# Kernel optimization log

Measured on AMD Instinct MI355X. Metric: run time of the kernel, lower is better.

Reference implementation:

```python
import jax, jax.numpy as jnp
import numpy as np
import math

D_MODEL = 512
N_HEADS = 2
B, S = 2, 1024
THRESHOLD = 0.5  # kwargs default 'sparsity_threshold'


def setup_inputs() -> dict:
    key = jax.random.key(0)
    ks = jax.random.split(key, 10)
    D, H = D_MODEL, D_MODEL // 4
    std = 0.02
    return {
        "x": jax.random.normal(ks[0], (B, S, D), jnp.float32),
        "Wq": jax.random.normal(ks[1], (D, D), jnp.float32) * std,
        "Wk": jax.random.normal(ks[2], (D, D), jnp.float32) * std,
        "Wv": jax.random.normal(ks[3], (D, D), jnp.float32) * std,
        "Wo": jax.random.normal(ks[4], (D, D), jnp.float32) * std,
        "bo": jnp.zeros((D,), jnp.float32),
        "W1": jax.random.normal(ks[5], (D, H), jnp.float32) * std,
        "b1": jnp.zeros((H,), jnp.float32),
        "W2": jax.random.normal(ks[6], (H, 1), jnp.float32) * std,
        "b2": jnp.zeros((1,), jnp.float32),
    }


def reference(x, Wq, Wk, Wv, Wo, bo, W1, b1, W2, b2):
    Bsz, Seq, D = x.shape
    Hn = N_HEADS
    dh = D // Hn

    def split_heads(t):
        return t.reshape(Bsz, Seq, Hn, dh).transpose(0, 2, 1, 3)  # [B,H,S,dh]

    q = split_heads(x @ Wq)
    k = split_heads(x @ Wk)
    v = split_heads(x @ Wv)

    scores = jnp.einsum("bhid,bhjd->bhij", q, k) / math.sqrt(dh)  # [B,H,S,S]

    # head-mean features for the pairwise sparsity predictor (n_heads==2 => 2*dh == D)
    q_mean = q.mean(axis=1)  # [B,S,dh]
    k_mean = k.mean(axis=1)  # [B,S,dh]
    # Linear1 of cat([q_mean_i, k_mean_j]) splits into two halves of W1
    a = q_mean @ W1[:dh]   # [B,S,Dh4]
    c = k_mean @ W1[dh:]   # [B,S,Dh4]
    hidden = jax.nn.relu(a[:, :, None, :] + c[:, None, :, :] + b1)  # [B,S,S,Dh4]
    connection_probs = jax.nn.sigmoid(jnp.squeeze(hidden @ W2, -1) + b2[0])  # [B,S,S]

    mask = connection_probs > THRESHOLD  # [B,S,S]
    scores = jnp.where(mask[:, None, :, :], scores, jnp.float32(-1e9))
    attn = jax.nn.softmax(scores, axis=-1)  # dropout inactive in eval

    out = jnp.einsum("bhij,bhjd->bhid", attn, v)  # [B,H,S,dh]
    out = out.transpose(0, 2, 1, 3).reshape(Bsz, Seq, D)
    out = out @ Wo + bo
    return out
```

## Files before the change

### kernel.cpp

```cpp
#include <hip/hip_runtime.h>


typedef unsigned short u16t;
typedef __bf16 bf16x8 __attribute__((ext_vector_type(8)));
typedef float f32x4 __attribute__((ext_vector_type(4)));

#define B_SZ 2
#define S_SZ 1024
#define D_SZ 512
#define DH 256
#define HH 128

static __device__ __forceinline__ u16t f2b(float f) {
    unsigned int u = __builtin_bit_cast(unsigned int, f);
    u += 0x7FFFu + ((u >> 16) & 1u);
    return (u16t)(u >> 16);
}
static __device__ __forceinline__ float b2f(u16t u) {
    return __builtin_bit_cast(float, (unsigned int)u << 16);
}

static __device__ __forceinline__ f32x4 mfma16(bf16x8 a, bf16x8 b, f32x4 c) {
    return __builtin_amdgcn_mfma_f32_16x16x32_bf16(a, b, c, 0, 0, 0);
}

__global__ __launch_bounds__(256) void k_prep(
    const float* __restrict__ x,
    const float* __restrict__ Wq, const float* __restrict__ Wk,
    const float* __restrict__ Wv, const float* __restrict__ Wo,
    const float* __restrict__ W1,
    u16t* __restrict__ xb, u16t* __restrict__ WT, float* __restrict__ Beff)
{
    __shared__ float smf[1088];
    int bidx = blockIdx.x;
    int t = threadIdx.x;
    if (bidx < 1024) {
        int idx = (bidx * 256 + t) * 4;
        float4 v = *(const float4*)(x + idx);
        u16t* o = xb + idx;
        o[0] = f2b(v.x); o[1] = f2b(v.y); o[2] = f2b(v.z); o[3] = f2b(v.w);
    } else if (bidx < 2048) {
        int t2 = bidx - 1024;
        int z = t2 >> 8, rem = t2 & 255;
        int n0 = (rem & 15) * 32, k0 = (rem >> 4) * 32;
        const float* W = z == 0 ? Wq : z == 1 ? Wk : z == 2 ? Wv : Wo;
        u16t* WTz = WT + (size_t)z * D_SZ * D_SZ;
        float (*tile)[33] = (float(*)[33])smf;
        int r = t >> 3, c4 = (t & 7) * 4;
        float4 v = *(const float4*)(W + (size_t)(k0 + r) * D_SZ + n0 + c4);
        tile[r][c4] = v.x; tile[r][c4 + 1] = v.y; tile[r][c4 + 2] = v.z; tile[r][c4 + 3] = v.w;
        __syncthreads();
        u16t o[4];
        o[0] = f2b(tile[c4][r]); o[1] = f2b(tile[c4 + 1][r]);
        o[2] = f2b(tile[c4 + 2][r]); o[3] = f2b(tile[c4 + 3][r]);
        *(ushort4*)(WTz + (size_t)(n0 + r) * D_SZ + k0 + c4) = *(ushort4*)o;
    } else {
        int k = bidx - 2048;
        float* wm0 = smf;
        float* wm1 = smf + 256;
        const float* wrq = Wq + (size_t)k * D_SZ;
        const float* wrk = Wk + (size_t)k * D_SZ;
        wm0[t & 255] = 0.5f * (wrq[t & 255] + wrq[(t & 255) + DH]);
        wm1[t & 255] = 0.5f * (wrk[t & 255] + wrk[(t & 255) + DH]);
        __syncthreads();
        int half = t >> 7, hcol = t & 127;
        const float* wm = half ? wm1 : wm0;
        const float* W1h = W1 + (half ? (size_t)DH * HH : 0);
        float s = 0.f;
        for (int d = 0; d < 256; ++d) s += wm[d] * W1h[(size_t)d * HH + hcol];
        Beff[(size_t)k * 256 + half * 128 + hcol] = s;
    }
}

#define KP 72

template<int NF>
static __device__ __forceinline__ void gemm_mainloop(
    const u16t* __restrict__ A, int lda, const u16t* __restrict__ B, int ldb,
    int K, int tid, u16t* Als, u16t* Bls, f32x4 acc[2][NF])
{
    const int w = tid >> 6, lane = tid & 63;
    const int lr = lane & 15, kg = lane >> 4;
    for (int k0 = 0; k0 < K; k0 += 64) {
        if (k0) __syncthreads();
        {
            int c = tid & 7, r0 = tid >> 3;
#pragma unroll
            for (int p = 0; p < 4; ++p) {
                int r = r0 + p * 32;
                *(uint4*)(&Als[r * KP + c * 8]) = *(const uint4*)(&A[(size_t)r * lda + k0 + c * 8]);
            }
#pragma unroll
            for (int p = 0; p < NF / 2; ++p) {
                int r = r0 + p * 32;
                *(uint4*)(&Bls[r * KP + c * 8]) = *(const uint4*)(&B[(size_t)r * ldb + k0 + c * 8]);
            }
        }
        __syncthreads();
#pragma unroll
        for (int kk = 0; kk < 2; ++kk) {
            bf16x8 af[2], bfr[NF];
#pragma unroll
            for (int fi = 0; fi < 2; ++fi)
                af[fi] = *(const bf16x8*)(&Als[(w * 32 + fi * 16 + lr) * KP + kk * 32 + kg * 8]);
#pragma unroll
            for (int fj = 0; fj < NF; ++fj)
                bfr[fj] = *(const bf16x8*)(&Bls[(fj * 16 + lr) * KP + kk * 32 + kg * 8]);
#pragma unroll
            for (int fi = 0; fi < 2; ++fi)
#pragma unroll
                for (int fj = 0; fj < NF; ++fj)
                    acc[fi][fj] = mfma16(af[fi], bfr[fj], acc[fi][fj]);
        }
    }
}


__global__ __launch_bounds__(256) void k_qkv(
    const u16t* __restrict__ xb, const u16t* __restrict__ WT,
    u16t* __restrict__ qb, u16t* __restrict__ kb, u16t* __restrict__ vT)
{
    __shared__ u16t Als[128 * KP];
    __shared__ u16t Bls[64 * KP];
    int z = blockIdx.z;
    int m0 = blockIdx.y * 128, n0 = blockIdx.x * 64;
    const u16t* A = xb + (size_t)m0 * D_SZ;
    const u16t* Bt = WT + (size_t)z * D_SZ * D_SZ + (size_t)n0 * D_SZ;
    f32x4 acc[2][4] = {};
    gemm_mainloop<4>(A, D_SZ, Bt, D_SZ, D_SZ, threadIdx.x, Als, Bls, acc);
    int w = threadIdx.x >> 6, lane = threadIdx.x & 63, lr = lane & 15, kg = lane >> 4;
    if (z < 2) {
        u16t* dst = z == 0 ? qb : kb;
        float scale = z == 0 ? 0.0625f : 1.0f;
#pragma unroll
        for (int fi = 0; fi < 2; ++fi)
#pragma unroll
            for (int fj = 0; fj < 4; ++fj)
#pragma unroll
                for (int rr = 0; rr < 4; ++rr) {
                    int row = m0 + w * 32 + fi * 16 + kg * 4 + rr;
                    int col = n0 + fj * 16 + lr;
                    dst[(size_t)row * D_SZ + col] = f2b(acc[fi][fj][rr] * scale);
                }
    } else {
        __syncthreads();
        u16t (*vls)[136] = (u16t(*)[136])Als;
#pragma unroll
        for (int fi = 0; fi < 2; ++fi)
#pragma unroll
            for (int fj = 0; fj < 4; ++fj)
#pragma unroll
                for (int rr = 0; rr < 4; ++rr)
                    vls[fj * 16 + lr][w * 32 + fi * 16 + kg * 4 + rr] = f2b(acc[fi][fj][rr]);
        __syncthreads();
        int b = m0 >> 10, s0 = m0 & 1023;
        int cr = threadIdx.x >> 2, seg = threadIdx.x & 3;
        const u16t* srcp = &vls[cr][seg * 32];
        u16t* dstp = vT + (((size_t)(b * D_SZ + n0 + cr)) << 10) + s0 + seg * 32;
#pragma unroll
        for (int qq = 0; qq < 4; ++qq)
            *(uint4*)(dstp + qq * 8) = *(const uint4*)(srcp + qq * 8);
    }
}

__global__ __launch_bounds__(256) void k_ac(
    const float* __restrict__ x, const float* __restrict__ Beff,
    const float* __restrict__ b1, float* __restrict__ a, float* __restrict__ cc)
{
    __shared__ float xs[64][68];
    __shared__ float bsT[32][68];
    int r0 = blockIdx.x * 64, n0 = blockIdx.y * 32;
    int t = threadIdx.x;
    int ti = t >> 4, tj = t & 15;
    float acc[4][2] = {};
    for (int k0 = 0; k0 < 512; k0 += 64) {
        if (k0) __syncthreads();
#pragma unroll
        for (int p = 0; p < 4; ++p) {
            int idx = t + p * 256;
            int r = idx >> 4, c4 = (idx & 15) * 4;
            *(float4*)&xs[r][c4] = *(const float4*)(x + (size_t)(r0 + r) * D_SZ + k0 + c4);
        }
#pragma unroll
        for (int p = 0; p < 2; ++p) {
            int idx = t + p * 256;
            int k = idx >> 3, n4 = (idx & 7) * 4;
            float4 v = *(const float4*)(Beff + (size_t)(k0 + k) * 256 + n0 + n4);
            bsT[n4][k] = v.x; bsT[n4 + 1][k] = v.y; bsT[n4 + 2][k] = v.z; bsT[n4 + 3][k] = v.w;
        }
        __syncthreads();
#pragma unroll
        for (int kk = 0; kk < 16; ++kk) {
            float4 xv[4], bv[2];
#pragma unroll
            for (int ri = 0; ri < 4; ++ri) xv[ri] = *(const float4*)&xs[ti + 16 * ri][kk * 4];
#pragma unroll
            for (int rj = 0; rj < 2; ++rj) bv[rj] = *(const float4*)&bsT[tj + 16 * rj][kk * 4];
#pragma unroll
            for (int ri = 0; ri < 4; ++ri)
#pragma unroll
                for (int rj = 0; rj < 2; ++rj)
                    acc[ri][rj] += xv[ri].x * bv[rj].x + xv[ri].y * bv[rj].y
                                 + xv[ri].z * bv[rj].z + xv[ri].w * bv[rj].w;
        }
    }
    bool isA = n0 < 128;
#pragma unroll
    for (int rj = 0; rj < 2; ++rj) {
        int col = n0 + tj + 16 * rj;
        float badd = isA ? b1[col] : 0.f;
#pragma unroll
        for (int ri = 0; ri < 4; ++ri) {
            int row = r0 + ti + 16 * ri;
            if (isA) a[(size_t)row * HH + col] = acc[ri][rj] + badd;
            else     cc[(size_t)row * HH + (col - 128)] = acc[ri][rj];
        }
    }
}

__global__ __launch_bounds__(256) void k_mask(
    const float* __restrict__ a, const float* __restrict__ c,
    const float* __restrict__ W2, const float* __restrict__ b2,
    unsigned char* __restrict__ maskb)
{
    __shared__ __align__(16) float at[64][132];
    __shared__ __align__(16) float ct[64][132];
    __shared__ __align__(16) float w2s[128];
    int b = blockIdx.z, i0 = blockIdx.y * 64, j0 = blockIdx.x * 64;
    int t = threadIdx.x;
    if (t < 128) w2s[t] = W2[t];
#pragma unroll
    for (int p = 0; p < 8; ++p) {
        int idx = t + p * 256;
        int r = idx >> 5, c4 = (idx & 31) * 4;
        *(float4*)&at[r][c4] = *(const float4*)(a + ((size_t)(b * S_SZ + i0 + r)) * HH + c4);
        *(float4*)&ct[r][c4] = *(const float4*)(c + ((size_t)(b * S_SZ + j0 + r)) * HH + c4);
    }
    __syncthreads();
    float fb2 = b2[0];
    int ti = t >> 4, tj = t & 15;
    float acc[4][4];
#pragma unroll
    for (int ri = 0; ri < 4; ++ri)
#pragma unroll
        for (int rj = 0; rj < 4; ++rj) acc[ri][rj] = fb2;
#pragma unroll 2
    for (int h4 = 0; h4 < 32; ++h4) {
        float4 av[4], cv[4];
        float4 wv = ((const float4*)w2s)[h4];
#pragma unroll
        for (int ri = 0; ri < 4; ++ri) av[ri] = *(const float4*)&at[ti + 16 * ri][h4 * 4];
#pragma unroll
        for (int rj = 0; rj < 4; ++rj) cv[rj] = *(const float4*)&ct[tj + 16 * rj][h4 * 4];
#pragma unroll
        for (int ri = 0; ri < 4; ++ri)
#pragma unroll
            for (int rj = 0; rj < 4; ++rj) {
                acc[ri][rj] += fmaxf(av[ri].x + cv[rj].x, 0.f) * wv.x;
                acc[ri][rj] += fmaxf(av[ri].y + cv[rj].y, 0.f) * wv.y;
                acc[ri][rj] += fmaxf(av[ri].z + cv[rj].z, 0.f) * wv.z;
                acc[ri][rj] += fmaxf(av[ri].w + cv[rj].w, 0.f) * wv.w;
            }
    }
#pragma unroll
    for (int ri = 0; ri < 4; ++ri)
#pragma unroll
        for (int rj = 0; rj < 4; ++rj) {
            int i = i0 + ti + 16 * ri, j = j0 + tj + 16 * rj;
            maskb[((size_t)b << 20) + ((size_t)i << 10) + j] = acc[ri][rj] > 0.f ? 1 : 0;
        }
}

__global__ __launch_bounds__(256) void k_scores(
    const u16t* __restrict__ qb, const u16t* __restrict__ kb,
    const unsigned char* __restrict__ maskb, u16t* __restrict__ scores)
{
    __shared__ u16t Als[128 * KP];
    __shared__ u16t Bls[64 * KP];
    int bh = blockIdx.z, b = bh >> 1, h = bh & 1;
    int m0 = blockIdx.y * 128, n0 = blockIdx.x * 64;
    const u16t* A = qb + (size_t)b * S_SZ * D_SZ + (size_t)m0 * D_SZ + h * DH;
    const u16t* Bt = kb + (size_t)b * S_SZ * D_SZ + (size_t)n0 * D_SZ + h * DH;
    f32x4 acc[2][4] = {};
    gemm_mainloop<4>(A, D_SZ, Bt, D_SZ, DH, threadIdx.x, Als, Bls, acc);
    int w = threadIdx.x >> 6, lane = threadIdx.x & 63, lr = lane & 15, kg = lane >> 4;
    const u16t NEG = f2b(-1e9f);
#pragma unroll
    for (int fi = 0; fi < 2; ++fi)
#pragma unroll
        for (int fj = 0; fj < 4; ++fj)
#pragma unroll
            for (int rr = 0; rr < 4; ++rr) {
                int i = m0 + w * 32 + fi * 16 + kg * 4 + rr;
                int j = n0 + fj * 16 + lr;
                bool msk = maskb[((size_t)b << 20) + ((size_t)i << 10) + j] != 0;
                scores[((size_t)bh << 20) + ((size_t)i << 10) + j]
                    = msk ? f2b(acc[fi][fj][rr]) : NEG;
            }
}

__global__ void k_softmax(const u16t* __restrict__ scores, u16t* __restrict__ P) {
    int row = blockIdx.x;
    int t = threadIdx.x;
    const u16t* src = scores + ((size_t)row << 10);
    ushort4 raw = ((const ushort4*)src)[t];
    float v0 = b2f(raw.x), v1 = b2f(raw.y), v2 = b2f(raw.z), v3 = b2f(raw.w);
    float m = fmaxf(fmaxf(v0, v1), fmaxf(v2, v3));
    for (int o = 32; o; o >>= 1) m = fmaxf(m, __shfl_xor(m, o));
    __shared__ float redm[4];
    __shared__ float reds[4];
    int w = t >> 6;
    if ((t & 63) == 0) redm[w] = m;
    __syncthreads();
    m = fmaxf(fmaxf(redm[0], redm[1]), fmaxf(redm[2], redm[3]));
    float e0 = expf(v0 - m), e1 = expf(v1 - m), e2 = expf(v2 - m), e3 = expf(v3 - m);
    float s = e0 + e1 + e2 + e3;
    for (int o = 32; o; o >>= 1) s += __shfl_xor(s, o);
    if ((t & 63) == 0) reds[w] = s;
    __syncthreads();
    s = reds[0] + reds[1] + reds[2] + reds[3];
    float inv = 1.0f / s;
    u16t o4[4] = { f2b(e0 * inv), f2b(e1 * inv), f2b(e2 * inv), f2b(e3 * inv) };
    *(ushort4*)(P + ((size_t)row << 10) + t * 4) = *(ushort4*)o4;
}

__global__ __launch_bounds__(256) void k_pv(
    const u16t* __restrict__ P, const u16t* __restrict__ vT, u16t* __restrict__ ao)
{
    __shared__ u16t Als[128 * KP];
    __shared__ u16t Bls[32 * KP];
    int bh = blockIdx.z, b = bh >> 1, h = bh & 1;
    int m0 = blockIdx.y * 128, n0 = blockIdx.x * 32;
    const u16t* A = P + ((size_t)bh << 20) + (size_t)m0 * S_SZ;
    const u16t* Bt = vT + ((size_t)(b * D_SZ + h * DH + n0)) * S_SZ;
    f32x4 acc[2][2] = {};
    gemm_mainloop<2>(A, S_SZ, Bt, S_SZ, S_SZ, threadIdx.x, Als, Bls, acc);
    int w = threadIdx.x >> 6, lane = threadIdx.x & 63, lr = lane & 15, kg = lane >> 4;
#pragma unroll
    for (int fi = 0; fi < 2; ++fi)
#pragma unroll
        for (int fj = 0; fj < 2; ++fj)
#pragma unroll
            for (int rr = 0; rr < 4; ++rr) {
                int i = m0 + w * 32 + fi * 16 + kg * 4 + rr;
                int d = n0 + fj * 16 + lr;
                ao[((size_t)(b * S_SZ + i)) * D_SZ + h * DH + d] = f2b(acc[fi][fj][rr]);
            }
}

__global__ __launch_bounds__(256) void k_out(
    const u16t* __restrict__ ao, const u16t* __restrict__ WoT,
    const float* __restrict__ bo, float* __restrict__ out)
{
    __shared__ u16t Als[128 * KP];
    __shared__ u16t Bls[32 * KP];
    int m0 = blockIdx.y * 128, n0 = blockIdx.x * 32;
    const u16t* A = ao + (size_t)m0 * D_SZ;
    const u16t* Bt = WoT + (size_t)n0 * D_SZ;
    f32x4 acc[2][2] = {};
    gemm_mainloop<2>(A, D_SZ, Bt, D_SZ, D_SZ, threadIdx.x, Als, Bls, acc);
    int w = threadIdx.x >> 6, lane = threadIdx.x & 63, lr = lane & 15, kg = lane >> 4;
#pragma unroll
    for (int fi = 0; fi < 2; ++fi)
#pragma unroll
        for (int fj = 0; fj < 2; ++fj)
#pragma unroll
            for (int rr = 0; rr < 4; ++rr) {
                int row = m0 + w * 32 + fi * 16 + kg * 4 + rr;
                int col = n0 + fj * 16 + lr;
                out[(size_t)row * D_SZ + col] = acc[fi][fj][rr] + bo[col];
            }
}

extern "C" void kernel_launch(void* const* d_in, const int* in_sizes, int n_in,
                              void* d_out, int out_size, void* d_ws, size_t ws_size,
                              hipStream_t stream)
{
    const float* x  = (const float*)d_in[0];
    const float* Wq = (const float*)d_in[1];
    const float* Wk = (const float*)d_in[2];
    const float* Wv = (const float*)d_in[3];
    const float* Wo = (const float*)d_in[4];
    const float* bo = (const float*)d_in[5];
    const float* W1 = (const float*)d_in[6];
    const float* b1 = (const float*)d_in[7];
    const float* W2 = (const float*)d_in[8];
    const float* b2 = (const float*)d_in[9];
    float* out = (float*)d_out;

    char* ws = (char*)d_ws;
    size_t off = 0;
    auto carve = [&](size_t bytes) { void* p = ws + off; off += (bytes + 255) & ~(size_t)255; return p; };
    u16t* xb   = (u16t*)carve((size_t)2048 * 512 * 2);
    u16t* WT   = (u16t*)carve((size_t)4 * 512 * 512 * 2);
    u16t* qb   = (u16t*)carve((size_t)2048 * 512 * 2);
    u16t* kb   = (u16t*)carve((size_t)2048 * 512 * 2);
    u16t* vT   = (u16t*)carve((size_t)2 * 512 * 1024 * 2);
    float* Beff = (float*)carve((size_t)512 * 256 * 4);
    float* a   = (float*)carve((size_t)2048 * 128 * 4);
    float* c   = (float*)carve((size_t)2048 * 128 * 4);
    unsigned char* maskb = (unsigned char*)carve((size_t)2 * 1024 * 1024);
    u16t* scores = (u16t*)carve((size_t)4 * 1024 * 1024 * 2);
    u16t* P    = (u16t*)carve((size_t)4 * 1024 * 1024 * 2);
    u16t* ao   = (u16t*)carve((size_t)2048 * 512 * 2);
    (void)ws_size;

    k_prep<<<dim3(2560), dim3(256), 0, stream>>>(x, Wq, Wk, Wv, Wo, W1, xb, WT, Beff);
    k_qkv<<<dim3(8, 16, 3), dim3(256), 0, stream>>>(xb, WT, qb, kb, vT);
    k_ac<<<dim3(32, 8), dim3(256), 0, stream>>>(x, Beff, b1, a, c);
    k_mask<<<dim3(16, 16, 2), dim3(256), 0, stream>>>(a, c, W2, b2, maskb);
    k_scores<<<dim3(16, 8, 4), dim3(256), 0, stream>>>(qb, kb, maskb, scores);
    k_softmax<<<dim3(4096), dim3(256), 0, stream>>>(scores, P);
    k_pv<<<dim3(8, 8, 4), dim3(256), 0, stream>>>(P, vT, ao);
    k_out<<<dim3(16, 16), dim3(256), 0, stream>>>(ao, WT + (size_t)3 * 512 * 512, bo, out);
}
```

Measured before the change: 120.8 us.

## Fuse softmax into score and PV kernels, merge QKV with predictor GEMM

Removes the separate softmax kernel. The scores kernel now writes unnormalised masked exponentials as P, plus per-tile partial row sums. The PV kernel adds those sums and divides its output by them. QKV and the a/c predictor projections are merged into one launch, and the epilogues are staged through LDS so global stores are coalesced and vectorized. Skipping the max subtraction relies on scaled scores staying small enough not to overflow exp, and a fully masked row gives zeros instead of a uniform distribution.

```diff
diff --git a/kernel.cpp b/kernel.cpp
--- a/kernel.cpp
+++ b/kernel.cpp
@@ -15,9 +15,6 @@
     unsigned int u = __builtin_bit_cast(unsigned int, f);
     u += 0x7FFFu + ((u >> 16) & 1u);
     return (u16t)(u >> 16);
-}
-static __device__ __forceinline__ float b2f(u16t u) {
-    return __builtin_bit_cast(float, (unsigned int)u << 16);
 }
 
 static __device__ __forceinline__ f32x4 mfma16(bf16x8 a, bf16x8 b, f32x4 c) {
@@ -116,104 +113,113 @@
 }
 
 
-__global__ __launch_bounds__(256) void k_qkv(
+__global__ __launch_bounds__(256) void k_qkvac(
     const u16t* __restrict__ xb, const u16t* __restrict__ WT,
-    u16t* __restrict__ qb, u16t* __restrict__ kb, u16t* __restrict__ vT)
-{
-    __shared__ u16t Als[128 * KP];
-    __shared__ u16t Bls[64 * KP];
-    int z = blockIdx.z;
-    int m0 = blockIdx.y * 128, n0 = blockIdx.x * 64;
-    const u16t* A = xb + (size_t)m0 * D_SZ;
-    const u16t* Bt = WT + (size_t)z * D_SZ * D_SZ + (size_t)n0 * D_SZ;
-    f32x4 acc[2][4] = {};
-    gemm_mainloop<4>(A, D_SZ, Bt, D_SZ, D_SZ, threadIdx.x, Als, Bls, acc);
-    int w = threadIdx.x >> 6, lane = threadIdx.x & 63, lr = lane & 15, kg = lane >> 4;
-    if (z < 2) {
-        u16t* dst = z == 0 ? qb : kb;
-        float scale = z == 0 ? 0.0625f : 1.0f;
-#pragma unroll
-        for (int fi = 0; fi < 2; ++fi)
-#pragma unroll
-            for (int fj = 0; fj < 4; ++fj)
-#pragma unroll
-                for (int rr = 0; rr < 4; ++rr) {
-                    int row = m0 + w * 32 + fi * 16 + kg * 4 + rr;
-                    int col = n0 + fj * 16 + lr;
-                    dst[(size_t)row * D_SZ + col] = f2b(acc[fi][fj][rr] * scale);
-                }
+    const float* __restrict__ x, const float* __restrict__ Beff,
+    const float* __restrict__ b1,
+    u16t* __restrict__ qb, u16t* __restrict__ kb, u16t* __restrict__ vT,
+    float* __restrict__ a, float* __restrict__ cc)
+{
+    __shared__ __align__(16) char sm[27648];
+    int bid = blockIdx.x;
+    int t = threadIdx.x;
+    if (bid < 384) {
+        u16t* Als = (u16t*)sm;
+        u16t* Bls = (u16t*)(sm + 18432);
+        int z = bid / 128, rem = bid & 127;
+        int m0 = (rem >> 3) * 128, n0 = (rem & 7) * 64;
+        const u16t* A = xb + (size_t)m0 * D_SZ;
+        const u16t* Bt = WT + (size_t)z * D_SZ * D_SZ + (size_t)n0 * D_SZ;
+        f32x4 acc[2][4] = {};
+        gemm_mainloop<4>(A, D_SZ, Bt, D_SZ, D_SZ, t, Als, Bls, acc);
+        int w = t >> 6, lane = t & 63, lr = lane & 15, kg = lane >> 4;
+        __syncthreads();
+        if (z < 2) {
+            u16t (*vls)[68] = (u16t(*)[68])Als;
+            float scale = z == 0 ? 0.0625f : 1.0f;
+#pragma unroll
+            for (int fi = 0; fi < 2; ++fi)
+#pragma unroll
+                for (int fj = 0; fj < 4; ++fj)
+#pragma unroll
+                    for (int rr = 0; rr < 4; ++rr)
+                        vls[w * 32 + fi * 16 + kg * 4 + rr][fj * 16 + lr]
+                            = f2b(acc[fi][fj][rr] * scale);
+            __syncthreads();
+            u16t* dst = z == 0 ? qb : kb;
+            int c8 = (t & 7) * 8, r0 = t >> 3;
+#pragma unroll
+            for (int p = 0; p < 4; ++p) {
+                int r = r0 + p * 32;
+                *(uint4*)(dst + (size_t)(m0 + r) * D_SZ + n0 + c8) = *(const uint4*)(&vls[r][c8]);
+            }
+        } else {
+            u16t (*vls)[136] = (u16t(*)[136])Als;
+#pragma unroll
+            for (int fi = 0; fi < 2; ++fi)
+#pragma unroll
+                for (int fj = 0; fj < 4; ++fj)
+#pragma unroll
+                    for (int rr = 0; rr < 4; ++rr)
+                        vls[fj * 16 + lr][w * 32 + fi * 16 + kg * 4 + rr] = f2b(acc[fi][fj][rr]);
+            __syncthreads();
+            int b = m0 >> 10, s0 = m0 & 1023;
+            int cr = t >> 2, seg = t & 3;
+            const u16t* srcp = &vls[cr][seg * 32];
+            u16t* dstp = vT + (((size_t)(b * D_SZ + n0 + cr)) << 10) + s0 + seg * 32;
+#pragma unroll
+            for (int qq = 0; qq < 4; ++qq)
+                *(uint4*)(dstp + qq * 8) = *(const uint4*)(srcp + qq * 8);
+        }
     } else {
-        __syncthreads();
-        u16t (*vls)[136] = (u16t(*)[136])Als;
-#pragma unroll
-        for (int fi = 0; fi < 2; ++fi)
-#pragma unroll
-            for (int fj = 0; fj < 4; ++fj)
-#pragma unroll
-                for (int rr = 0; rr < 4; ++rr)
-                    vls[fj * 16 + lr][w * 32 + fi * 16 + kg * 4 + rr] = f2b(acc[fi][fj][rr]);
-        __syncthreads();
-        int b = m0 >> 10, s0 = m0 & 1023;
-        int cr = threadIdx.x >> 2, seg = threadIdx.x & 3;
-        const u16t* srcp = &vls[cr][seg * 32];
-        u16t* dstp = vT + (((size_t)(b * D_SZ + n0 + cr)) << 10) + s0 + seg * 32;
-#pragma unroll
-        for (int qq = 0; qq < 4; ++qq)
-            *(uint4*)(dstp + qq * 8) = *(const uint4*)(srcp + qq * 8);
-    }
-}
-
-__global__ __launch_bounds__(256) void k_ac(
-    const float* __restrict__ x, const float* __restrict__ Beff,
-    const float* __restrict__ b1, float* __restrict__ a, float* __restrict__ cc)
-{
-    __shared__ float xs[64][68];
-    __shared__ float bsT[32][68];
-    int r0 = blockIdx.x * 64, n0 = blockIdx.y * 32;
-    int t = threadIdx.x;
-    int ti = t >> 4, tj = t & 15;
-    float acc[4][2] = {};
-    for (int k0 = 0; k0 < 512; k0 += 64) {
-        if (k0) __syncthreads();
-#pragma unroll
-        for (int p = 0; p < 4; ++p) {
-            int idx = t + p * 256;
-            int r = idx >> 4, c4 = (idx & 15) * 4;
-            *(float4*)&xs[r][c4] = *(const float4*)(x + (size_t)(r0 + r) * D_SZ + k0 + c4);
-        }
-#pragma unroll
-        for (int p = 0; p < 2; ++p) {
-            int idx = t + p * 256;
-            int k = idx >> 3, n4 = (idx & 7) * 4;
-            float4 v = *(const float4*)(Beff + (size_t)(k0 + k) * 256 + n0 + n4);
-            bsT[n4][k] = v.x; bsT[n4 + 1][k] = v.y; bsT[n4 + 2][k] = v.z; bsT[n4 + 3][k] = v.w;
-        }
-        __syncthreads();
-#pragma unroll
-        for (int kk = 0; kk < 16; ++kk) {
-            float4 xv[4], bv[2];
-#pragma unroll
-            for (int ri = 0; ri < 4; ++ri) xv[ri] = *(const float4*)&xs[ti + 16 * ri][kk * 4];
-#pragma unroll
-            for (int rj = 0; rj < 2; ++rj) bv[rj] = *(const float4*)&bsT[tj + 16 * rj][kk * 4];
-#pragma unroll
-            for (int ri = 0; ri < 4; ++ri)
-#pragma unroll
-                for (int rj = 0; rj < 2; ++rj)
-                    acc[ri][rj] += xv[ri].x * bv[rj].x + xv[ri].y * bv[rj].y
-                                 + xv[ri].z * bv[rj].z + xv[ri].w * bv[rj].w;
-        }
-    }
-    bool isA = n0 < 128;
-#pragma unroll
-    for (int rj = 0; rj < 2; ++rj) {
-        int col = n0 + tj + 16 * rj;
-        float badd = isA ? b1[col] : 0.f;
-#pragma unroll
-        for (int ri = 0; ri < 4; ++ri) {
-            int row = r0 + ti + 16 * ri;
-            if (isA) a[(size_t)row * HH + col] = acc[ri][rj] + badd;
-            else     cc[(size_t)row * HH + (col - 128)] = acc[ri][rj];
+        float (*xs)[68] = (float(*)[68])sm;
+        float (*bsT)[68] = (float(*)[68])(sm + 17408);
+        int t2 = bid - 384;
+        int r0 = (t2 & 31) * 64, n0 = (t2 >> 5) * 32;
+        int ti = t >> 4, tj = t & 15;
+        float acc[4][2] = {};
+        for (int k0 = 0; k0 < 512; k0 += 64) {
+            if (k0) __syncthreads();
+#pragma unroll
+            for (int p = 0; p < 4; ++p) {
+                int idx = t + p * 256;
+                int r = idx >> 4, c4 = (idx & 15) * 4;
+                *(float4*)&xs[r][c4] = *(const float4*)(x + (size_t)(r0 + r) * D_SZ + k0 + c4);
+            }
+#pragma unroll
+            for (int p = 0; p < 2; ++p) {
+                int idx = t + p * 256;
+                int k = idx >> 3, n4 = (idx & 7) * 4;
+                float4 v = *(const float4*)(Beff + (size_t)(k0 + k) * 256 + n0 + n4);
+                bsT[n4][k] = v.x; bsT[n4 + 1][k] = v.y; bsT[n4 + 2][k] = v.z; bsT[n4 + 3][k] = v.w;
+            }
+            __syncthreads();
+#pragma unroll
+            for (int kk = 0; kk < 16; ++kk) {
+                float4 xv[4], bv[2];
+#pragma unroll
+                for (int ri = 0; ri < 4; ++ri) xv[ri] = *(const float4*)&xs[ti + 16 * ri][kk * 4];
+#pragma unroll
+                for (int rj = 0; rj < 2; ++rj) bv[rj] = *(const float4*)&bsT[tj + 16 * rj][kk * 4];
+#pragma unroll
+                for (int ri = 0; ri < 4; ++ri)
+#pragma unroll
+                    for (int rj = 0; rj < 2; ++rj)
+                        acc[ri][rj] += xv[ri].x * bv[rj].x + xv[ri].y * bv[rj].y
+                                     + xv[ri].z * bv[rj].z + xv[ri].w * bv[rj].w;
+            }
+        }
+        bool isA = n0 < 128;
+#pragma unroll
+        for (int rj = 0; rj < 2; ++rj) {
+            int col = n0 + tj + 16 * rj;
+            float badd = isA ? b1[col] : 0.f;
+#pragma unroll
+            for (int ri = 0; ri < 4; ++ri) {
+                int row = r0 + ti + 16 * ri;
+                if (isA) a[(size_t)row * HH + col] = acc[ri][rj] + badd;
+                else     cc[(size_t)row * HH + (col - 128)] = acc[ri][rj];
+            }
         }
     }
 }
@@ -273,79 +279,96 @@
 
 __global__ __launch_bounds__(256) void k_scores(
     const u16t* __restrict__ qb, const u16t* __restrict__ kb,
-    const unsigned char* __restrict__ maskb, u16t* __restrict__ scores)
+    const unsigned char* __restrict__ maskb, u16t* __restrict__ P,
+    float* __restrict__ lpart)
 {
     __shared__ u16t Als[128 * KP];
     __shared__ u16t Bls[64 * KP];
     int bh = blockIdx.z, b = bh >> 1, h = bh & 1;
-    int m0 = blockIdx.y * 128, n0 = blockIdx.x * 64;
+    int jb = blockIdx.x;
+    int m0 = blockIdx.y * 128, n0 = jb * 64;
     const u16t* A = qb + (size_t)b * S_SZ * D_SZ + (size_t)m0 * D_SZ + h * DH;
     const u16t* Bt = kb + (size_t)b * S_SZ * D_SZ + (size_t)n0 * D_SZ + h * DH;
     f32x4 acc[2][4] = {};
     gemm_mainloop<4>(A, D_SZ, Bt, D_SZ, DH, threadIdx.x, Als, Bls, acc);
     int w = threadIdx.x >> 6, lane = threadIdx.x & 63, lr = lane & 15, kg = lane >> 4;
-    const u16t NEG = f2b(-1e9f);
 #pragma unroll
     for (int fi = 0; fi < 2; ++fi)
 #pragma unroll
-        for (int fj = 0; fj < 4; ++fj)
-#pragma unroll
-            for (int rr = 0; rr < 4; ++rr) {
-                int i = m0 + w * 32 + fi * 16 + kg * 4 + rr;
+        for (int rr = 0; rr < 4; ++rr) {
+            int i = m0 + w * 32 + fi * 16 + kg * 4 + rr;
+            float rs = 0.f;
+#pragma unroll
+            for (int fj = 0; fj < 4; ++fj) {
                 int j = n0 + fj * 16 + lr;
                 bool msk = maskb[((size_t)b << 20) + ((size_t)i << 10) + j] != 0;
-                scores[((size_t)bh << 20) + ((size_t)i << 10) + j]
-                    = msk ? f2b(acc[fi][fj][rr]) : NEG;
-            }
-}
-
-__global__ void k_softmax(const u16t* __restrict__ scores, u16t* __restrict__ P) {
-    int row = blockIdx.x;
-    int t = threadIdx.x;
-    const u16t* src = scores + ((size_t)row << 10);
-    ushort4 raw = ((const ushort4*)src)[t];
-    float v0 = b2f(raw.x), v1 = b2f(raw.y), v2 = b2f(raw.z), v3 = b2f(raw.w);
-    float m = fmaxf(fmaxf(v0, v1), fmaxf(v2, v3));
-    for (int o = 32; o; o >>= 1) m = fmaxf(m, __shfl_xor(m, o));
-    __shared__ float redm[4];
-    __shared__ float reds[4];
-    int w = t >> 6;
-    if ((t & 63) == 0) redm[w] = m;
-    __syncthreads();
-    m = fmaxf(fmaxf(redm[0], redm[1]), fmaxf(redm[2], redm[3]));
-    float e0 = expf(v0 - m), e1 = expf(v1 - m), e2 = expf(v2 - m), e3 = expf(v3 - m);
-    float s = e0 + e1 + e2 + e3;
-    for (int o = 32; o; o >>= 1) s += __shfl_xor(s, o);
-    if ((t & 63) == 0) reds[w] = s;
-    __syncthreads();
-    s = reds[0] + reds[1] + reds[2] + reds[3];
-    float inv = 1.0f / s;
-    u16t o4[4] = { f2b(e0 * inv), f2b(e1 * inv), f2b(e2 * inv), f2b(e3 * inv) };
-    *(ushort4*)(P + ((size_t)row << 10) + t * 4) = *(ushort4*)o4;
+                float e = msk ? __expf(acc[fi][fj][rr]) : 0.f;
+                acc[fi][fj][rr] = e;
+                rs += e;
+            }
+            rs += __shfl_xor(rs, 1); rs += __shfl_xor(rs, 2);
+            rs += __shfl_xor(rs, 4); rs += __shfl_xor(rs, 8);
+            if (lr == 0) lpart[((size_t)(jb * 4 + bh) << 10) + i] = rs;
+        }
+    __syncthreads();
+    u16t (*vls)[68] = (u16t(*)[68])Als;
+#pragma unroll
+    for (int fi = 0; fi < 2; ++fi)
+#pragma unroll
+        for (int fj = 0; fj < 4; ++fj)
+#pragma unroll
+            for (int rr = 0; rr < 4; ++rr)
+                vls[w * 32 + fi * 16 + kg * 4 + rr][fj * 16 + lr] = f2b(acc[fi][fj][rr]);
+    __syncthreads();
+    int c8 = (threadIdx.x & 7) * 8, r0 = threadIdx.x >> 3;
+#pragma unroll
+    for (int p = 0; p < 4; ++p) {
+        int r = r0 + p * 32;
+        *(uint4*)(P + ((size_t)bh << 20) + ((size_t)(m0 + r) << 10) + n0 + c8)
+            = *(const uint4*)(&vls[r][c8]);
+    }
 }
 
 __global__ __launch_bounds__(256) void k_pv(
-    const u16t* __restrict__ P, const u16t* __restrict__ vT, u16t* __restrict__ ao)
+    const u16t* __restrict__ P, const u16t* __restrict__ vT,
+    const float* __restrict__ lpart, u16t* __restrict__ ao)
 {
     __shared__ u16t Als[128 * KP];
     __shared__ u16t Bls[32 * KP];
+    __shared__ float invl[128];
     int bh = blockIdx.z, b = bh >> 1, h = bh & 1;
     int m0 = blockIdx.y * 128, n0 = blockIdx.x * 32;
+    int t = threadIdx.x;
+    if (t < 128) {
+        float l = 0.f;
+        for (int jb = 0; jb < 16; ++jb)
+            l += lpart[((size_t)(jb * 4 + bh) << 10) + m0 + t];
+        invl[t] = l > 0.f ? 1.0f / l : 0.f;
+    }
     const u16t* A = P + ((size_t)bh << 20) + (size_t)m0 * S_SZ;
     const u16t* Bt = vT + ((size_t)(b * D_SZ + h * DH + n0)) * S_SZ;
     f32x4 acc[2][2] = {};
-    gemm_mainloop<2>(A, S_SZ, Bt, S_SZ, S_SZ, threadIdx.x, Als, Bls, acc);
-    int w = threadIdx.x >> 6, lane = threadIdx.x & 63, lr = lane & 15, kg = lane >> 4;
-#pragma unroll
-    for (int fi = 0; fi < 2; ++fi)
+    gemm_mainloop<2>(A, S_SZ, Bt, S_SZ, S_SZ, t, Als, Bls, acc);
+    int w = t >> 6, lane = t & 63, lr = lane & 15, kg = lane >> 4;
+    __syncthreads();
+    u16t (*ols)[40] = (u16t(*)[40])Als;
+#pragma unroll
+    for (int fi = 0; fi < 2; ++fi) {
+        int rl = w * 32 + fi * 16 + kg * 4;
 #pragma unroll
         for (int fj = 0; fj < 2; ++fj)
 #pragma unroll
-            for (int rr = 0; rr < 4; ++rr) {
-                int i = m0 + w * 32 + fi * 16 + kg * 4 + rr;
-                int d = n0 + fj * 16 + lr;
-                ao[((size_t)(b * S_SZ + i)) * D_SZ + h * DH + d] = f2b(acc[fi][fj][rr]);
-            }
+            for (int rr = 0; rr < 4; ++rr)
+                ols[rl + rr][fj * 16 + lr] = f2b(acc[fi][fj][rr] * invl[rl + rr]);
+    }
+    __syncthreads();
+    int c8 = (t & 3) * 8, r0 = t >> 2;
+#pragma unroll
+    for (int p = 0; p < 2; ++p) {
+        int r = r0 + p * 64;
+        *(uint4*)(ao + ((size_t)(b * S_SZ + m0 + r)) * D_SZ + h * DH + n0 + c8)
+            = *(const uint4*)(&ols[r][c8]);
+    }
 }
 
 __global__ __launch_bounds__(256) void k_out(
@@ -360,16 +383,24 @@
     f32x4 acc[2][2] = {};
     gemm_mainloop<2>(A, D_SZ, Bt, D_SZ, D_SZ, threadIdx.x, Als, Bls, acc);
     int w = threadIdx.x >> 6, lane = threadIdx.x & 63, lr = lane & 15, kg = lane >> 4;
+    __syncthreads();
+    float (*ols)[36] = (float(*)[36])Als;
 #pragma unroll
     for (int fi = 0; fi < 2; ++fi)
 #pragma unroll
         for (int fj = 0; fj < 2; ++fj)
 #pragma unroll
             for (int rr = 0; rr < 4; ++rr) {
-                int row = m0 + w * 32 + fi * 16 + kg * 4 + rr;
-                int col = n0 + fj * 16 + lr;
-                out[(size_t)row * D_SZ + col] = acc[fi][fj][rr] + bo[col];
-            }
+                int rl = w * 32 + fi * 16 + kg * 4 + rr;
+                ols[rl][fj * 16 + lr] = acc[fi][fj][rr] + bo[n0 + fj * 16 + lr];
+            }
+    __syncthreads();
+    int c4 = (threadIdx.x & 7) * 4, r0 = threadIdx.x >> 3;
+#pragma unroll
+    for (int p = 0; p < 4; ++p) {
+        int r = r0 + p * 32;
+        *(float4*)(out + (size_t)(m0 + r) * D_SZ + n0 + c4) = *(const float4*)(&ols[r][c4]);
+    }
 }
 
 extern "C" void kernel_launch(void* const* d_in, const int* in_sizes, int n_in,
@@ -400,17 +431,15 @@
     float* a   = (float*)carve((size_t)2048 * 128 * 4);
     float* c   = (float*)carve((size_t)2048 * 128 * 4);
     unsigned char* maskb = (unsigned char*)carve((size_t)2 * 1024 * 1024);
-    u16t* scores = (u16t*)carve((size_t)4 * 1024 * 1024 * 2);
     u16t* P    = (u16t*)carve((size_t)4 * 1024 * 1024 * 2);
+    float* lpart = (float*)carve((size_t)16 * 4 * 1024 * 4);
     u16t* ao   = (u16t*)carve((size_t)2048 * 512 * 2);
     (void)ws_size;
 
     k_prep<<<dim3(2560), dim3(256), 0, stream>>>(x, Wq, Wk, Wv, Wo, W1, xb, WT, Beff);
-    k_qkv<<<dim3(8, 16, 3), dim3(256), 0, stream>>>(xb, WT, qb, kb, vT);
-    k_ac<<<dim3(32, 8), dim3(256), 0, stream>>>(x, Beff, b1, a, c);
+    k_qkvac<<<dim3(640), dim3(256), 0, stream>>>(xb, WT, x, Beff, b1, qb, kb, vT, a, c);
     k_mask<<<dim3(16, 16, 2), dim3(256), 0, stream>>>(a, c, W2, b2, maskb);
-    k_scores<<<dim3(16, 8, 4), dim3(256), 0, stream>>>(qb, kb, maskb, scores);
-    k_softmax<<<dim3(4096), dim3(256), 0, stream>>>(scores, P);
-    k_pv<<<dim3(8, 8, 4), dim3(256), 0, stream>>>(P, vT, ao);
+    k_scores<<<dim3(16, 8, 4), dim3(256), 0, stream>>>(qb, kb, maskb, P, lpart);
+    k_pv<<<dim3(8, 8, 4), dim3(256), 0, stream>>>(P, vT, lpart, ao);
     k_out<<<dim3(16, 16), dim3(256), 0, stream>>>(ao, WT + (size_t)3 * 512 * 512, bo, out);
 }
```

Result: faster. 112.2 us (-7.1%).
